# Kernel optimization log

Hardware: AMD Instinct MI355X
Metric: run time of the kernel (lower is better)

Reference implementation:

```python
import jax, jax.numpy as jnp
import numpy as np
import math

B, C, H, W = 16, 64, 128, 128
EPS = 1e-5


def _ln(x, g, b):
    m = jnp.mean(x, axis=-1, keepdims=True)
    v = jnp.var(x, axis=-1, keepdims=True)
    return (x - m) * jax.lax.rsqrt(v + EPS) * g + b


def setup_inputs() -> dict:
    key = jax.random.key(0)
    ks = jax.random.split(key, 8)
    s = 1.0 / math.sqrt(C)
    return {
        "x_l": jax.random.normal(ks[0], (B, C, H, W), dtype=jnp.float32),
        "x_h": jax.random.normal(ks[1], (B, C, H, W), dtype=jnp.float32),
        "ln1_g": jnp.ones((C,), jnp.float32),
        "ln1_b": jnp.zeros((C,), jnp.float32),
        "ln2_g": jnp.ones((C,), jnp.float32),
        "ln2_b": jnp.zeros((C,), jnp.float32),
        "Wq": jax.random.normal(ks[2], (C, C), dtype=jnp.float32) * s,
        "Wk": jax.random.normal(ks[3], (C, C), dtype=jnp.float32) * s,
        "Wv1": jax.random.normal(ks[4], (C, C), dtype=jnp.float32) * s,
        "Wv2": jax.random.normal(ks[5], (C, C), dtype=jnp.float32) * s,
    }


def reference(x_l, x_h, ln1_g, ln1_b, ln2_g, ln2_b, Wq, Wk, Wv1, Wv2):
    # [B,C,H,W] -> [B,H,W,C]
    xl = jnp.transpose(x_l, (0, 2, 3, 1))
    xh = jnp.transpose(x_h, (0, 2, 3, 1))
    # torch Linear: x @ W.T (no bias)
    xl_v = xl @ Wv1.T
    xh_v = xh @ Wv2.T
    q = _ln(xl, ln1_g, ln1_b) @ Wq.T
    k = _ln(xh, ln2_g, ln2_b) @ Wk.T
    # shared score matrix over the W axis: [B,H,W,W]
    attn = jnp.einsum('bhwc,bhvc->bhwv', q, k) * (1.0 / math.sqrt(C))
    attn_h = jax.nn.softmax(attn, axis=-1)                                  # row softmax
    attn_l = jax.nn.softmax(jnp.swapaxes(attn, 2, 3), axis=-1)              # column softmax
    xl_o = jnp.einsum('bhwv,bhvc->bhwc', attn_l, xl_v)
    xh_o = jnp.einsum('bhwv,bhvc->bhwc', attn_h, xh_v)
    xh_out = xh + xl_o
    xl_out = xl + xh_o
    # back to [B,C,H,W]
    return (jnp.transpose(xl_out, (0, 3, 1, 2)), jnp.transpose(xh_out, (0, 3, 1, 2)))
```

## Files before the change

kernel.cpp:

```cpp
#include <hip/hip_runtime.h>
#include <cstdint>


typedef __attribute__((ext_vector_type(8))) short bf16x8;
typedef __attribute__((ext_vector_type(4))) float f32x4;
typedef __attribute__((ext_vector_type(2))) unsigned u32x2;

#define LAM 0.18033688011112042f

__device__ __forceinline__ unsigned rne_hi(float x) {
  unsigned u = __float_as_uint(x);
  return (u + 0x7FFFu + ((u >> 16) & 1u)) >> 16;
}
__device__ __forceinline__ void split2(float x, unsigned short& h, unsigned short& l) {
  unsigned hb = rne_hi(x);
  float rf = x - __uint_as_float(hb << 16);
  h = (unsigned short)hb;
  l = (unsigned short)(__float_as_uint(rf) >> 16);
}
__device__ __forceinline__ unsigned split_pack(float x) {
  unsigned short h, l; split2(x, h, l);
  return ((unsigned)h << 16) | (unsigned)l;
}
__device__ __forceinline__ float unpack_f(unsigned p) {
  return __uint_as_float(p & 0xFFFF0000u) + __uint_as_float(p << 16);
}
__device__ __forceinline__ f32x4 mm3(bf16x8 ah, bf16x8 al, bf16x8 bh, bf16x8 bl, f32x4 c) {
  c = __builtin_amdgcn_mfma_f32_16x16x32_bf16(al, bh, c, 0, 0, 0);
  c = __builtin_amdgcn_mfma_f32_16x16x32_bf16(ah, bl, c, 0, 0, 0);
  c = __builtin_amdgcn_mfma_f32_16x16x32_bf16(ah, bh, c, 0, 0, 0);
  return c;
}
__device__ __forceinline__ void row_frag(const unsigned* p, bf16x8& fh, bf16x8& fl) {
  u32x2 q0 = *(const u32x2*)p, q1 = *(const u32x2*)(p + 2);
  u32x2 q2 = *(const u32x2*)(p + 4), q3 = *(const u32x2*)(p + 6);
  unsigned w0 = q0[0], w1 = q0[1], w2 = q1[0], w3 = q1[1];
  unsigned w4 = q2[0], w5 = q2[1], w6 = q3[0], w7 = q3[1];
  fh[0] = (short)(w0 >> 16); fl[0] = (short)(w0 & 0xFFFFu);
  fh[1] = (short)(w1 >> 16); fl[1] = (short)(w1 & 0xFFFFu);
  fh[2] = (short)(w2 >> 16); fl[2] = (short)(w2 & 0xFFFFu);
  fh[3] = (short)(w3 >> 16); fl[3] = (short)(w3 & 0xFFFFu);
  fh[4] = (short)(w4 >> 16); fl[4] = (short)(w4 & 0xFFFFu);
  fh[5] = (short)(w5 >> 16); fl[5] = (short)(w5 & 0xFFFFu);
  fh[6] = (short)(w6 >> 16); fl[6] = (short)(w6 & 0xFFFFu);
  fh[7] = (short)(w7 >> 16); fl[7] = (short)(w7 & 0xFFFFu);
}

__global__ void scam_prepack(const float* __restrict__ ln1g, const float* __restrict__ ln1b,
                             const float* __restrict__ ln2g, const float* __restrict__ ln2b,
                             const float* __restrict__ Wq, const float* __restrict__ Wk,
                             const float* __restrict__ Wv1, const float* __restrict__ Wv2,
                             unsigned short* __restrict__ WP, float* __restrict__ vecs) {
  __shared__ float Wkl[64][65];
  __shared__ float wqc[64][4];
  __shared__ float gb[4][64];
  const int tid = threadIdx.x;
  const int blk = blockIdx.x;
  const int c0 = blk * 4;
#pragma unroll
  for (int i = 0; i < 16; ++i) {
    int idx = i * 256 + tid;
    Wkl[idx >> 6][idx & 63] = Wk[idx];
  }
  { int o = tid >> 2, ci = tid & 3; wqc[o][ci] = Wq[o * 64 + c0 + ci]; }
  { int g = tid >> 6, e = tid & 63;
    const float* src = (g == 0) ? ln1g : (g == 1) ? ln1b : (g == 2) ? ln2g : ln2b;
    gb[g][e] = src[e]; }
  __syncthreads();
  const int ci = tid >> 6, cp = tid & 63;
  const int c = c0 + ci;
  float d = 0.f;
#pragma unroll 8
  for (int o = 0; o < 64; ++o) d += wqc[o][ci] * Wkl[o][cp];
  d *= LAM;
  float mb = gb[0][c] * d * gb[2][cp];
  float tb = gb[1][c] * d * gb[2][cp];
  atomicAdd(&vecs[cp], mb);
  atomicAdd(&vecs[64 + cp], tb);
  {
    unsigned short h, l; split2(mb, h, l);
    int nt = cp >> 4, l15 = cp & 15, ks = c >> 5, lg = (c >> 3) & 3, j = c & 7;
    int ui = (nt * 2 + ks) * 512 + (lg * 16 + l15) * 8 + j;
    WP[ui] = h; WP[4096 + ui] = l;
  }
  float t = d * gb[3][cp];
#pragma unroll
  for (int s = 1; s < 64; s <<= 1) t += __shfl_xor(t, s);
  if ((tid & 63) == 0) {
    vecs[128 + c] = gb[0][c] * t;
    atomicAdd(&vecs[192], gb[0][c] * t);
    atomicAdd(&vecs[193], gb[1][c] * t);
  }
  int idx2 = blk * 256 + tid;
#pragma unroll
  for (int m = 0; m < 2; ++m) {
    float v = (m ? Wv2 : Wv1)[idx2];
    unsigned short h, l; split2(v, h, l);
    int o = idx2 >> 6, cc = idx2 & 63;
    int mt = o >> 4, l15 = o & 15, ks = cc >> 5, lg = (cc >> 3) & 3, j = cc & 7;
    int ui = m * 8192 + (mt * 2 + ks) * 512 + (lg * 16 + l15) * 8 + j;
    WP[8192 + ui] = h;
    WP[8192 + ui + 4096] = l;
  }
}

struct SMem {
  unsigned X[2][64][130];
  union {
    unsigned short T2[2][128][72];
    unsigned E[128][130];
    unsigned short O[2][2][128][72];
  } R;
  float m_[2][128], r_[2][128];
  float uT[128], vT[128], zr[128], zc[128];
  float vT2[2][128];
  float zrP[2][128];
  float zcP[8][128];
  float s1v[64], t1v[64], mbv[64];
  float smbv, tmbv;
};

__launch_bounds__(1024, 1)
__global__ void scam_main(const float* __restrict__ xl_g, const float* __restrict__ xh_g,
                          const unsigned short* __restrict__ WP, const float* __restrict__ vecs,
                          float* __restrict__ out) {
  __shared__ __align__(16) SMem sm;
  const int tid = threadIdx.x;
  const int lane = tid & 63;
  const int wid = tid >> 6;
  const int stripe = wid >> 1, chalf = wid & 1;
  const int l15 = lane & 15, lg = lane >> 4;
  const int s = blockIdx.x;
  const size_t xoff = (size_t)(s >> 7) * 1048576u + (size_t)(s & 127) * 128u;

  {
    float* Z = &sm.vT2[0][0];
    for (int i = tid; i < 1536; i += 1024) Z[i] = 0.f;
    if (tid < 64) {
      sm.s1v[tid] = vecs[tid];
      sm.t1v[tid] = vecs[64 + tid];
      sm.mbv[tid] = vecs[128 + tid];
    }
    if (tid == 64) { sm.smbv = vecs[192]; sm.tmbv = vecs[193]; }
    const int q = tid & 31, cb = tid >> 5;
#pragma unroll
    for (int i = 0; i < 4; ++i) {
      int mat = i >> 1, c = cb + (i & 1) * 32;
      const float* xg = mat ? xh_g : xl_g;
      f32x4 v = *(const f32x4*)(xg + xoff + (size_t)c * 16384u + q * 4);
      u32x2 p0, p1;
      p0[0] = split_pack(v[0]); p0[1] = split_pack(v[1]);
      p1[0] = split_pack(v[2]); p1[1] = split_pack(v[3]);
      *(u32x2*)&sm.X[mat][c][q * 4] = p0;
      *(u32x2*)&sm.X[mat][c][q * 4 + 2] = p1;
    }
  }
  __syncthreads();

  {
    const int row = tid >> 2, qu = tid & 3;
    const int mat = row >> 7, w = row & 127;
    float a1 = 0.f, a2 = 0.f, a3 = 0.f;
#pragma unroll
    for (int i = 0; i < 16; ++i) {
      int c = qu + i * 4;
      float x = unpack_f(sm.X[mat][c][w]);
      a1 += x; a2 += x * x;
      if (mat == 0) a3 += x * sm.mbv[c];
    }
    a1 += __shfl_xor(a1, 1); a2 += __shfl_xor(a2, 1); a3 += __shfl_xor(a3, 1);
    a1 += __shfl_xor(a1, 2); a2 += __shfl_xor(a2, 2); a3 += __shfl_xor(a3, 2);
    if (qu == 0) {
      float mn = a1 * (1.f / 64.f);
      float var = fmaxf(a2 * (1.f / 64.f) - mn * mn, 0.f);
      float rs = rsqrtf(var + 1e-5f);
      sm.m_[mat][w] = mn; sm.r_[mat][w] = rs;
      if (mat == 0) sm.uT[w] = rs * (a3 - mn * sm.smbv) + sm.tmbv;
    }
  }
  __syncthreads();

  {
    const int wA = stripe * 16 + l15;
    bf16x8 Ah[2], Al[2];
#pragma unroll
    for (int ks = 0; ks < 2; ++ks)
#pragma unroll
      for (int j = 0; j < 8; ++j) {
        unsigned p = sm.X[0][ks * 32 + lg * 8 + j][wA];
        Ah[ks][j] = (short)(p >> 16); Al[ks][j] = (short)(p & 0xFFFFu);
      }
    f32x4 acc[2];
#pragma unroll
    for (int nt = 0; nt < 2; ++nt)
#pragma unroll
      for (int r = 0; r < 4; ++r) acc[nt][r] = 0.f;
#pragma unroll
    for (int nt = 0; nt < 2; ++nt) {
      int ntg = chalf * 2 + nt;
#pragma unroll
      for (int ks = 0; ks < 2; ++ks) {
        const unsigned short* wp = WP + (ntg * 2 + ks) * 512 + lane * 8;
        bf16x8 Bh = *(const bf16x8*)wp;
        bf16x8 Bl = *(const bf16x8*)(wp + 4096);
        acc[nt] = mm3(Ah[ks], Al[ks], Bh, Bl, acc[nt]);
      }
    }
    float vsum[4] = {0.f, 0.f, 0.f, 0.f};
#pragma unroll
    for (int nt = 0; nt < 2; ++nt) {
      int cp = (chalf * 2 + nt) * 16 + l15;
      float sv = sm.s1v[cp], tv = sm.t1v[cp];
#pragma unroll
      for (int r = 0; r < 4; ++r) {
        int wr = stripe * 16 + lg * 4 + r;
        float t2 = sm.r_[0][wr] * (acc[nt][r] - sm.m_[0][wr] * sv) + tv;
        unsigned short h, l; split2(t2, h, l);
        sm.R.T2[0][wr][cp] = h; sm.R.T2[1][wr][cp] = l;
        vsum[r] += t2;
      }
    }
#pragma unroll
    for (int r = 0; r < 4; ++r) {
      float v = vsum[r];
      v += __shfl_xor(v, 1); v += __shfl_xor(v, 2);
      v += __shfl_xor(v, 4); v += __shfl_xor(v, 8);
      if (l15 == 0) sm.vT2[chalf][stripe * 16 + lg * 4 + r] = v;
    }
  }
  __syncthreads();

  {
    if (tid < 128) sm.vT[tid] = sm.vT2[0][tid] + sm.vT2[1][tid];
    const int wA = stripe * 16 + l15;
    bf16x8 Ah[2], Al[2];
#pragma unroll
    for (int ks = 0; ks < 2; ++ks) {
      Ah[ks] = *(const bf16x8*)&sm.R.T2[0][wA][ks * 32 + lg * 8];
      Al[ks] = *(const bf16x8*)&sm.R.T2[1][wA][ks * 32 + lg * 8];
    }
    f32x4 acc[4];
#pragma unroll
    for (int nt = 0; nt < 4; ++nt)
#pragma unroll
      for (int r = 0; r < 4; ++r) acc[nt][r] = 0.f;
#pragma unroll
    for (int nt = 0; nt < 4; ++nt) {
      int wk = (chalf * 4 + nt) * 16 + l15;
#pragma unroll
      for (int ks = 0; ks < 2; ++ks) {
        bf16x8 Bh, Bl;
#pragma unroll
        for (int j = 0; j < 8; ++j) {
          unsigned p = sm.X[1][ks * 32 + lg * 8 + j][wk];
          Bh[j] = (short)(p >> 16); Bl[j] = (short)(p & 0xFFFFu);
        }
        acc[nt] = mm3(Ah[ks], Al[ks], Bh, Bl, acc[nt]);
      }
    }
    __syncthreads();
    float ev[4][4];
#pragma unroll
    for (int nt = 0; nt < 4; ++nt) {
      int wk = (chalf * 4 + nt) * 16 + l15;
      float rr = sm.r_[1][wk], mm = sm.m_[1][wk];
#pragma unroll
      for (int r = 0; r < 4; ++r) {
        int wq = stripe * 16 + lg * 4 + r;
        float s2 = rr * (acc[nt][r] - mm * sm.vT[wq]) + sm.uT[wq];
        float e = __builtin_amdgcn_exp2f(s2);
        ev[nt][r] = e;
        sm.R.E[wq][wk] = split_pack(e);
      }
    }
#pragma unroll
    for (int r = 0; r < 4; ++r) {
      float v = ev[0][r] + ev[1][r] + ev[2][r] + ev[3][r];
      v += __shfl_xor(v, 1); v += __shfl_xor(v, 2);
      v += __shfl_xor(v, 4); v += __shfl_xor(v, 8);
      if (l15 == 0) sm.zrP[chalf][stripe * 16 + lg * 4 + r] = v;
    }
#pragma unroll
    for (int nt = 0; nt < 4; ++nt) {
      float v = ev[nt][0] + ev[nt][1] + ev[nt][2] + ev[nt][3];
      v += __shfl_xor(v, 16); v += __shfl_xor(v, 32);
      if (lg == 0) sm.zcP[stripe][(chalf * 4 + nt) * 16 + l15] = v;
    }
  }
  __syncthreads();

  {
    if (tid < 128) {
      sm.zr[tid] = 1.0f / (sm.zrP[0][tid] + sm.zrP[1][tid]);
    } else if (tid < 256) {
      int c = tid - 128;
      float t = 0.f;
#pragma unroll
      for (int st = 0; st < 8; ++st) t += sm.zcP[st][c];
      sm.zc[c] = 1.0f / t;
    }
    const int wA = stripe * 16 + l15;
    f32x4 aH[2], aL[2];
#pragma unroll
    for (int nt = 0; nt < 2; ++nt)
#pragma unroll
      for (int r = 0; r < 4; ++r) { aH[nt][r] = 0.f; aL[nt][r] = 0.f; }
#pragma unroll
    for (int kt = 0; kt < 4; ++kt) {
      bf16x8 Eh, El;
      row_frag(&sm.R.E[wA][kt * 32 + lg * 8], Eh, El);
      bf16x8 Th, Tl;
#pragma unroll
      for (int j = 0; j < 8; ++j) {
        unsigned p = sm.R.E[kt * 32 + lg * 8 + j][wA];
        Th[j] = (short)(p >> 16); Tl[j] = (short)(p & 0xFFFFu);
      }
#pragma unroll
      for (int nt = 0; nt < 2; ++nt) {
        int c = (chalf * 2 + nt) * 16 + l15;
        bf16x8 BHh, BHl, BLh, BLl;
        row_frag(&sm.X[1][c][kt * 32 + lg * 8], BHh, BHl);
        row_frag(&sm.X[0][c][kt * 32 + lg * 8], BLh, BLl);
        aH[nt] = mm3(Eh, El, BHh, BHl, aH[nt]);
        aL[nt] = mm3(Th, Tl, BLh, BLl, aL[nt]);
      }
    }
    __syncthreads();
#pragma unroll
    for (int nt = 0; nt < 2; ++nt) {
      int c = (chalf * 2 + nt) * 16 + l15;
#pragma unroll
      for (int r = 0; r < 4; ++r) {
        int w = stripe * 16 + lg * 4 + r;
        unsigned short h, l;
        split2(aH[nt][r] * sm.zr[w], h, l);
        sm.R.O[0][0][w][c] = h; sm.R.O[0][1][w][c] = l;
        split2(aL[nt][r] * sm.zc[w], h, l);
        sm.R.O[1][0][w][c] = h; sm.R.O[1][1][w][c] = l;
      }
    }
  }
  __syncthreads();

  {
    const int mt = wid >> 2, np = wid & 3;
#pragma unroll
    for (int oi = 0; oi < 2; ++oi) {
      const int osel = oi;
      const int wsel = oi ? 0 : 1;
      const unsigned short* WA = WP + 8192 + wsel * 8192;
      bf16x8 Ah[2], Al[2];
#pragma unroll
      for (int ks = 0; ks < 2; ++ks) {
        const unsigned short* wp = WA + (mt * 2 + ks) * 512 + lane * 8;
        Ah[ks] = *(const bf16x8*)wp;
        Al[ks] = *(const bf16x8*)(wp + 4096);
      }
      f32x4 acc[2];
#pragma unroll
      for (int nt2 = 0; nt2 < 2; ++nt2)
#pragma unroll
        for (int r = 0; r < 4; ++r) acc[nt2][r] = 0.f;
#pragma unroll
      for (int nt2 = 0; nt2 < 2; ++nt2) {
        int wc = (np * 2 + nt2) * 16 + l15;
#pragma unroll
        for (int ks = 0; ks < 2; ++ks) {
          bf16x8 Bh = *(const bf16x8*)&sm.R.O[osel][0][wc][ks * 32 + lg * 8];
          bf16x8 Bl = *(const bf16x8*)&sm.R.O[osel][1][wc][ks * 32 + lg * 8];
          acc[nt2] = mm3(Ah[ks], Al[ks], Bh, Bl, acc[nt2]);
        }
      }
      const float* res = (oi ? xh_g : xl_g) + xoff;
      float* og = out + (size_t)oi * 16777216u + xoff;
#pragma unroll
      for (int nt2 = 0; nt2 < 2; ++nt2) {
        int wc = (np * 2 + nt2) * 16 + l15;
#pragma unroll
        for (int r = 0; r < 4; ++r) {
          int o = mt * 16 + lg * 4 + r;
          size_t a = (size_t)o * 16384u + wc;
          og[a] = acc[nt2][r] + res[a];
        }
      }
    }
  }
}

extern "C" void kernel_launch(void* const* d_in, const int* in_sizes, int n_in,
                              void* d_out, int out_size, void* d_ws, size_t ws_size,
                              hipStream_t stream) {
  (void)in_sizes; (void)n_in; (void)out_size; (void)ws_size;
  unsigned short* WP = (unsigned short*)d_ws;
  float* vecs = (float*)((char*)d_ws + 49152);
  hipMemsetAsync(vecs, 0, 1024, stream);
  scam_prepack<<<16, 256, 0, stream>>>(
      (const float*)d_in[2], (const float*)d_in[3],
      (const float*)d_in[4], (const float*)d_in[5],
      (const float*)d_in[6], (const float*)d_in[7],
      (const float*)d_in[8], (const float*)d_in[9], WP, vecs);
  scam_main<<<2048, 1024, 0, stream>>>(
      (const float*)d_in[0], (const float*)d_in[1], WP, vecs, (float*)d_out);
}
```

Before: 354.9 us.

## Split packed hi/lo shared buffers into swizzled bf16 planes for direct fragment loads

Replaces the shared-memory layout that packed each value's bf16 hi and lo halves into one 32-bit word with separate hi and lo bf16 planes. The X and E planes are indexed through an XOR swizzle that keeps 8-element groups contiguous. Row-oriented MFMA fragments can then be read with single 16-byte loads instead of four 8-byte loads followed by shift and mask unpacking. This is meant to cut LDS instruction count, unpack ALU work and bank conflicts. The cost is that column-wise (transposed) gathers now need two 16-bit reads per element where one 32-bit read served before. The global input loads are also hoisted ahead of the parameter-vector loads, and the zero-init loop over vT2/zrP/zcP is dropped, which is only safe if those arrays are fully overwritten before they are read.

Result: slower. 381.6 us (+7.5%).

```diff
diff --git a/kernel.cpp b/kernel.cpp
--- a/kernel.cpp
+++ b/kernel.cpp
@@ -4,9 +4,11 @@
 
 typedef __attribute__((ext_vector_type(8))) short bf16x8;
 typedef __attribute__((ext_vector_type(4))) float f32x4;
-typedef __attribute__((ext_vector_type(2))) unsigned u32x2;
+typedef __attribute__((ext_vector_type(4))) unsigned short u16x4;
 
 #define LAM 0.18033688011112042f
+
+__device__ __forceinline__ int XSW(int r, int c) { return (r * 136 + c) ^ (r & 56); }
 
 __device__ __forceinline__ unsigned rne_hi(float x) {
   unsigned u = __float_as_uint(x);
@@ -18,32 +20,14 @@
   h = (unsigned short)hb;
   l = (unsigned short)(__float_as_uint(rf) >> 16);
 }
-__device__ __forceinline__ unsigned split_pack(float x) {
-  unsigned short h, l; split2(x, h, l);
-  return ((unsigned)h << 16) | (unsigned)l;
-}
-__device__ __forceinline__ float unpack_f(unsigned p) {
-  return __uint_as_float(p & 0xFFFF0000u) + __uint_as_float(p << 16);
+__device__ __forceinline__ float comb(unsigned short h, unsigned short l) {
+  return __uint_as_float((unsigned)h << 16) + __uint_as_float((unsigned)l << 16);
 }
 __device__ __forceinline__ f32x4 mm3(bf16x8 ah, bf16x8 al, bf16x8 bh, bf16x8 bl, f32x4 c) {
   c = __builtin_amdgcn_mfma_f32_16x16x32_bf16(al, bh, c, 0, 0, 0);
   c = __builtin_amdgcn_mfma_f32_16x16x32_bf16(ah, bl, c, 0, 0, 0);
   c = __builtin_amdgcn_mfma_f32_16x16x32_bf16(ah, bh, c, 0, 0, 0);
   return c;
-}
-__device__ __forceinline__ void row_frag(const unsigned* p, bf16x8& fh, bf16x8& fl) {
-  u32x2 q0 = *(const u32x2*)p, q1 = *(const u32x2*)(p + 2);
-  u32x2 q2 = *(const u32x2*)(p + 4), q3 = *(const u32x2*)(p + 6);
-  unsigned w0 = q0[0], w1 = q0[1], w2 = q1[0], w3 = q1[1];
-  unsigned w4 = q2[0], w5 = q2[1], w6 = q3[0], w7 = q3[1];
-  fh[0] = (short)(w0 >> 16); fl[0] = (short)(w0 & 0xFFFFu);
-  fh[1] = (short)(w1 >> 16); fl[1] = (short)(w1 & 0xFFFFu);
-  fh[2] = (short)(w2 >> 16); fl[2] = (short)(w2 & 0xFFFFu);
-  fh[3] = (short)(w3 >> 16); fl[3] = (short)(w3 & 0xFFFFu);
-  fh[4] = (short)(w4 >> 16); fl[4] = (short)(w4 & 0xFFFFu);
-  fh[5] = (short)(w5 >> 16); fl[5] = (short)(w5 & 0xFFFFu);
-  fh[6] = (short)(w6 >> 16); fl[6] = (short)(w6 & 0xFFFFu);
-  fh[7] = (short)(w7 >> 16); fl[7] = (short)(w7 & 0xFFFFu);
 }
 
 __global__ void scam_prepack(const float* __restrict__ ln1g, const float* __restrict__ ln1b,
@@ -105,17 +89,15 @@
 }
 
 struct SMem {
-  unsigned X[2][64][130];
+  unsigned short X[2][2][8704];
   union {
-    unsigned short T2[2][128][72];
-    unsigned E[128][130];
-    unsigned short O[2][2][128][72];
+    unsigned short T2[2][9216];
+    unsigned short E[2][17408];
+    unsigned short O[2][2][9216];
   } R;
   float m_[2][128], r_[2][128];
   float uT[128], vT[128], zr[128], zc[128];
-  float vT2[2][128];
-  float zrP[2][128];
-  float zcP[8][128];
+  float vT2[2][128], zrP[2][128], zcP[8][128];
   float s1v[64], t1v[64], mbv[64];
   float smbv, tmbv;
 };
@@ -134,25 +116,29 @@
   const size_t xoff = (size_t)(s >> 7) * 1048576u + (size_t)(s & 127) * 128u;
 
   {
-    float* Z = &sm.vT2[0][0];
-    for (int i = tid; i < 1536; i += 1024) Z[i] = 0.f;
+    const int q = tid & 31, cb = tid >> 5;
+    f32x4 v[4];
+#pragma unroll
+    for (int i = 0; i < 4; ++i) {
+      int mat = i >> 1, c = cb + (i & 1) * 32;
+      const float* xg = mat ? xh_g : xl_g;
+      v[i] = *(const f32x4*)(xg + xoff + (size_t)c * 16384u + q * 4);
+    }
     if (tid < 64) {
       sm.s1v[tid] = vecs[tid];
       sm.t1v[tid] = vecs[64 + tid];
       sm.mbv[tid] = vecs[128 + tid];
     }
     if (tid == 64) { sm.smbv = vecs[192]; sm.tmbv = vecs[193]; }
-    const int q = tid & 31, cb = tid >> 5;
 #pragma unroll
     for (int i = 0; i < 4; ++i) {
       int mat = i >> 1, c = cb + (i & 1) * 32;
-      const float* xg = mat ? xh_g : xl_g;
-      f32x4 v = *(const f32x4*)(xg + xoff + (size_t)c * 16384u + q * 4);
-      u32x2 p0, p1;
-      p0[0] = split_pack(v[0]); p0[1] = split_pack(v[1]);
-      p1[0] = split_pack(v[2]); p1[1] = split_pack(v[3]);
-      *(u32x2*)&sm.X[mat][c][q * 4] = p0;
-      *(u32x2*)&sm.X[mat][c][q * 4 + 2] = p1;
+      u16x4 h4, l4;
+#pragma unroll
+      for (int j = 0; j < 4; ++j) { unsigned short hh, ll; split2(v[i][j], hh, ll); h4[j] = hh; l4[j] = ll; }
+      int idx = XSW(c, q * 4);
+      *(u16x4*)&sm.X[mat][0][idx] = h4;
+      *(u16x4*)&sm.X[mat][1][idx] = l4;
     }
   }
   __syncthreads();
@@ -163,8 +149,9 @@
     float a1 = 0.f, a2 = 0.f, a3 = 0.f;
 #pragma unroll
     for (int i = 0; i < 16; ++i) {
-      int c = qu + i * 4;
-      float x = unpack_f(sm.X[mat][c][w]);
+      int c = qu * 16 + i;
+      int idx = XSW(c, w);
+      float x = comb(sm.X[mat][0][idx], sm.X[mat][1][idx]);
       a1 += x; a2 += x * x;
       if (mat == 0) a3 += x * sm.mbv[c];
     }
@@ -187,8 +174,9 @@
     for (int ks = 0; ks < 2; ++ks)
 #pragma unroll
       for (int j = 0; j < 8; ++j) {
-        unsigned p = sm.X[0][ks * 32 + lg * 8 + j][wA];
-        Ah[ks][j] = (short)(p >> 16); Al[ks][j] = (short)(p & 0xFFFFu);
+        int idx = XSW(ks * 32 + lg * 8 + j, wA);
+        Ah[ks][j] = (short)sm.X[0][0][idx];
+        Al[ks][j] = (short)sm.X[0][1][idx];
       }
     f32x4 acc[2];
 #pragma unroll
@@ -216,7 +204,8 @@
         int wr = stripe * 16 + lg * 4 + r;
         float t2 = sm.r_[0][wr] * (acc[nt][r] - sm.m_[0][wr] * sv) + tv;
         unsigned short h, l; split2(t2, h, l);
-        sm.R.T2[0][wr][cp] = h; sm.R.T2[1][wr][cp] = l;
+        sm.R.T2[0][wr * 72 + cp] = h;
+        sm.R.T2[1][wr * 72 + cp] = l;
         vsum[r] += t2;
       }
     }
@@ -236,8 +225,8 @@
     bf16x8 Ah[2], Al[2];
 #pragma unroll
     for (int ks = 0; ks < 2; ++ks) {
-      Ah[ks] = *(const bf16x8*)&sm.R.T2[0][wA][ks * 32 + lg * 8];
-      Al[ks] = *(const bf16x8*)&sm.R.T2[1][wA][ks * 32 + lg * 8];
+      Ah[ks] = *(const bf16x8*)&sm.R.T2[0][wA * 72 + ks * 32 + lg * 8];
+      Al[ks] = *(const bf16x8*)&sm.R.T2[1][wA * 72 + ks * 32 + lg * 8];
     }
     f32x4 acc[4];
 #pragma unroll
@@ -252,8 +241,9 @@
         bf16x8 Bh, Bl;
 #pragma unroll
         for (int j = 0; j < 8; ++j) {
-          unsigned p = sm.X[1][ks * 32 + lg * 8 + j][wk];
-          Bh[j] = (short)(p >> 16); Bl[j] = (short)(p & 0xFFFFu);
+          int idx = XSW(ks * 32 + lg * 8 + j, wk);
+          Bh[j] = (short)sm.X[1][0][idx];
+          Bl[j] = (short)sm.X[1][1][idx];
         }
         acc[nt] = mm3(Ah[ks], Al[ks], Bh, Bl, acc[nt]);
       }
@@ -270,7 +260,10 @@
         float s2 = rr * (acc[nt][r] - mm * sm.vT[wq]) + sm.uT[wq];
         float e = __builtin_amdgcn_exp2f(s2);
         ev[nt][r] = e;
-        sm.R.E[wq][wk] = split_pack(e);
+        unsigned short h, l; split2(e, h, l);
+        int idx = XSW(wq, wk);
+        sm.R.E[0][idx] = h;
+        sm.R.E[1][idx] = l;
       }
     }
 #pragma unroll
@@ -307,20 +300,23 @@
       for (int r = 0; r < 4; ++r) { aH[nt][r] = 0.f; aL[nt][r] = 0.f; }
 #pragma unroll
     for (int kt = 0; kt < 4; ++kt) {
-      bf16x8 Eh, El;
-      row_frag(&sm.R.E[wA][kt * 32 + lg * 8], Eh, El);
+      bf16x8 Eh = *(const bf16x8*)&sm.R.E[0][XSW(wA, kt * 32 + lg * 8)];
+      bf16x8 El = *(const bf16x8*)&sm.R.E[1][XSW(wA, kt * 32 + lg * 8)];
       bf16x8 Th, Tl;
 #pragma unroll
       for (int j = 0; j < 8; ++j) {
-        unsigned p = sm.R.E[kt * 32 + lg * 8 + j][wA];
-        Th[j] = (short)(p >> 16); Tl[j] = (short)(p & 0xFFFFu);
+        int idx = XSW(kt * 32 + lg * 8 + j, wA);
+        Th[j] = (short)sm.R.E[0][idx];
+        Tl[j] = (short)sm.R.E[1][idx];
       }
 #pragma unroll
       for (int nt = 0; nt < 2; ++nt) {
         int c = (chalf * 2 + nt) * 16 + l15;
-        bf16x8 BHh, BHl, BLh, BLl;
-        row_frag(&sm.X[1][c][kt * 32 + lg * 8], BHh, BHl);
-        row_frag(&sm.X[0][c][kt * 32 + lg * 8], BLh, BLl);
+        int bidx = XSW(c, kt * 32 + lg * 8);
+        bf16x8 BHh = *(const bf16x8*)&sm.X[1][0][bidx];
+        bf16x8 BHl = *(const bf16x8*)&sm.X[1][1][bidx];
+        bf16x8 BLh = *(const bf16x8*)&sm.X[0][0][bidx];
+        bf16x8 BLl = *(const bf16x8*)&sm.X[0][1][bidx];
         aH[nt] = mm3(Eh, El, BHh, BHl, aH[nt]);
         aL[nt] = mm3(Th, Tl, BLh, BLl, aL[nt]);
       }
@@ -334,9 +330,11 @@
         int w = stripe * 16 + lg * 4 + r;
         unsigned short h, l;
         split2(aH[nt][r] * sm.zr[w], h, l);
-        sm.R.O[0][0][w][c] = h; sm.R.O[0][1][w][c] = l;
+        sm.R.O[0][0][w * 72 + c] = h;
+        sm.R.O[0][1][w * 72 + c] = l;
         split2(aL[nt][r] * sm.zc[w], h, l);
-        sm.R.O[1][0][w][c] = h; sm.R.O[1][1][w][c] = l;
+        sm.R.O[1][0][w * 72 + c] = h;
+        sm.R.O[1][1][w * 72 + c] = l;
       }
     }
   }
@@ -366,8 +364,8 @@
         int wc = (np * 2 + nt2) * 16 + l15;
 #pragma unroll
         for (int ks = 0; ks < 2; ++ks) {
-          bf16x8 Bh = *(const bf16x8*)&sm.R.O[osel][0][wc][ks * 32 + lg * 8];
-          bf16x8 Bl = *(const bf16x8*)&sm.R.O[osel][1][wc][ks * 32 + lg * 8];
+          bf16x8 Bh = *(const bf16x8*)&sm.R.O[osel][0][wc * 72 + ks * 32 + lg * 8];
+          bf16x8 Bl = *(const bf16x8*)&sm.R.O[osel][1][wc * 72 + ks * 32 + lg * 8];
           acc[nt2] = mm3(Ah[ks], Al[ks], Bh, Bl, acc[nt2]);
         }
       }
```
